# Performance work log

Measured on AMD Instinct MI355X. Metric: run time of the kernel, lower is better.

Reference implementation:

```python
import jax, jax.numpy as jnp
import numpy as np

D_MODEL = 1024
NUM_HEADS = 16
D_HEAD = D_MODEL // NUM_HEADS
BATCH, SEQ, MEM = 2, 1024, 1024
TOT = SEQ + MEM


def setup_inputs() -> dict:
    key = jax.random.key(0)
    ks = jax.random.split(key, 16)
    s = 0.02
    return {
        "x": jax.random.normal(ks[0], (BATCH, SEQ, D_MODEL), jnp.float32),
        "mem": jax.random.normal(ks[1], (BATCH, MEM, D_MODEL), jnp.float32),
        "mask": jnp.zeros((1, 1, SEQ, TOT), jnp.float32),
        "rel_enc": jax.random.normal(ks[2], (TOT, D_MODEL), jnp.float32),
        "Wq": jax.random.normal(ks[3], (D_MODEL, D_MODEL), jnp.float32) * s,
        "bq": jnp.zeros((D_MODEL,), jnp.float32),
        "Wke": jax.random.normal(ks[4], (D_MODEL, D_MODEL), jnp.float32) * s,
        "bke": jnp.zeros((D_MODEL,), jnp.float32),
        "Wkr": jax.random.normal(ks[5], (D_MODEL, D_MODEL), jnp.float32) * s,
        "bkr": jnp.zeros((D_MODEL,), jnp.float32),
        "Wv": jax.random.normal(ks[6], (D_MODEL, D_MODEL), jnp.float32) * s,
        "bv": jnp.zeros((D_MODEL,), jnp.float32),
        "Wo": jax.random.normal(ks[7], (D_MODEL, D_MODEL), jnp.float32) * s,
        "bo": jnp.zeros((D_MODEL,), jnp.float32),
    }


def _split_heads(t, b):
    # (b, s, d_model) -> (b, h, s, d_head)
    return t.reshape(b, -1, NUM_HEADS, D_HEAD).transpose(0, 2, 1, 3)


def _rel_enc_shift(arr):
    # arr: (b, h, l, m) -> Transformer-XL shift trick
    b, h, l, m = arr.shape
    arr = jnp.concatenate([arr, jnp.zeros((b, h, l, 1), arr.dtype)], axis=-1)
    arr = arr.reshape(b, h, l * (m + 1))
    return arr[:, :, l - 1:-1].reshape(b, h, l, m)


def reference(x, mem, mask, rel_enc, Wq, bq, Wke, bke, Wkr, bkr, Wv, bv, Wo, bo):
    b, s, _ = x.shape
    x_tilde = jnp.concatenate([mem, x], axis=1)  # (b, tot, d)
    q = _split_heads(x @ Wq + bq, b)             # (b, h, s, dh)
    k = _split_heads(x_tilde @ Wke + bke, b)     # (b, h, tot, dh)
    v = _split_heads(x_tilde @ Wv + bv, b)       # (b, h, tot, dh)
    A = jnp.einsum("bhsd,bhtd->bhst", q, k)      # content scores
    Q = (rel_enc @ Wkr + bkr).reshape(-1, NUM_HEADS, D_HEAD).transpose(1, 0, 2)  # (h, tot, dh)
    B_hat = jnp.einsum("bhsd,htd->bhst", q, Q)
    B = _rel_enc_shift(B_hat)                    # relative-position scores
    scores = (A + B) / jnp.sqrt(jnp.float32(D_HEAD)) + mask * -1e9
    w = jax.nn.softmax(scores, axis=-1)
    out = jnp.einsum("bhst,bhtd->bhsd", w, v)
    out = out.transpose(0, 2, 1, 3).reshape(b, s, D_MODEL)
    return out @ Wo + bo
```

## Files before the change

kernel.cpp:

```cpp
#include <hip/hip_runtime.h>

typedef unsigned short ushort;
typedef unsigned int uint;
typedef __attribute__((ext_vector_type(8))) short short8;
typedef __attribute__((ext_vector_type(4))) float float4v;

#define D_MODEL 1024
#define NH 16
#define DH 64
#define BATCH 2
#define SEQ 1024
#define MEMLEN 1024
#define TOT 2048

__device__ __forceinline__ float b2f(ushort u) {
  return __uint_as_float(((uint)u) << 16);
}
__device__ __forceinline__ ushort f2b(float f) {
  uint i = __float_as_uint(f);
  uint r = (i + 0x7fffu + ((i >> 16) & 1u)) >> 16;
  return (ushort)r;
}
__device__ __forceinline__ void gld16(const ushort* g, ushort* l) {
  __builtin_amdgcn_global_load_lds(
      (const __attribute__((address_space(1))) void*)g,
      (__attribute__((address_space(3))) void*)l, 16, 0, 0);
}

__global__ __launch_bounds__(256) void concat_cvt_kernel(
    const float* __restrict__ x, const float* __restrict__ mem,
    ushort* __restrict__ xt, ushort* __restrict__ xb) {
  int idx = blockIdx.x * 256 + threadIdx.x;
  int row = idx >> 7;
  int c8 = (idx & 127) << 3;
  int b = row >> 11;
  int i = row & 2047;
  const float* src = (i < MEMLEN) ? &mem[((b << 10) + i) * D_MODEL]
                                  : &x[((b << 10) + (i - MEMLEN)) * D_MODEL];
  float4 f0 = *(const float4*)(&src[c8]);
  float4 f1 = *(const float4*)(&src[c8 + 4]);
  ushort u[8] = {f2b(f0.x), f2b(f0.y), f2b(f0.z), f2b(f0.w),
                 f2b(f1.x), f2b(f1.y), f2b(f1.z), f2b(f1.w)};
  *(uint4*)(&xt[row * D_MODEL + c8]) = *(const uint4*)u;
  if (i >= MEMLEN)
    *(uint4*)(&xb[((b << 10) + (i - MEMLEN)) * D_MODEL + c8]) = *(const uint4*)u;
}

__global__ __launch_bounds__(256) void cvt_kernel(const float* __restrict__ in,
                                                  ushort* __restrict__ out) {
  int idx = blockIdx.x * 256 + threadIdx.x;
  int base = idx << 3;
  float4 f0 = *(const float4*)(&in[base]);
  float4 f1 = *(const float4*)(&in[base + 4]);
  ushort u[8] = {f2b(f0.x), f2b(f0.y), f2b(f0.z), f2b(f0.w),
                 f2b(f1.x), f2b(f1.y), f2b(f1.z), f2b(f1.w)};
  *(uint4*)(&out[base]) = *(const uint4*)u;
}

__global__ __launch_bounds__(256) void maskcvt_kernel(
    const float* __restrict__ in, ushort* __restrict__ out) {
  int idx = blockIdx.x * 256 + threadIdx.x;
  int base = idx << 3;
  float4 f0 = *(const float4*)(&in[base]);
  float4 f1 = *(const float4*)(&in[base + 4]);
  ushort u[8] = {f2b(f0.x * -1e9f), f2b(f0.y * -1e9f), f2b(f0.z * -1e9f),
                 f2b(f0.w * -1e9f), f2b(f1.x * -1e9f), f2b(f1.y * -1e9f),
                 f2b(f1.z * -1e9f), f2b(f1.w * -1e9f)};
  *(uint4*)(&out[base]) = *(const uint4*)u;
}

__global__ __launch_bounds__(256) void transpose_cvt5_kernel(
    const float* __restrict__ W0, const float* __restrict__ W1,
    const float* __restrict__ W2, const float* __restrict__ W3,
    const float* __restrict__ W4, ushort* __restrict__ T0,
    ushort* __restrict__ T1, ushort* __restrict__ T2, ushort* __restrict__ T3,
    ushort* __restrict__ T4) {
  __shared__ ushort tle[32][33];
  const float* W;
  ushort* T;
  switch (blockIdx.z) {
    case 0: W = W0; T = T0; break;
    case 1: W = W1; T = T1; break;
    case 2: W = W2; T = T2; break;
    case 3: W = W3; T = T3; break;
    default: W = W4; T = T4; break;
  }
  const int bx = blockIdx.x * 32, by = blockIdx.y * 32;
  const int tx = threadIdx.x & 31, ty = threadIdx.x >> 5;
#pragma unroll
  for (int j = 0; j < 32; j += 8)
    tle[ty + j][tx] = f2b(W[(by + ty + j) * 1024 + bx + tx]);
  __syncthreads();
#pragma unroll
  for (int j = 0; j < 32; j += 8)
    T[(bx + ty + j) * 1024 + by + tx] = tle[tx][ty + j];
}

__global__ __launch_bounds__(256) void vtrans_kernel(
    const ushort* __restrict__ kv, ushort* __restrict__ vt) {
  __shared__ ushort tle[32][76];
  const int gx = blockIdx.x;
  const int gy = blockIdx.y;
  const int tid = threadIdx.x;
  const int r = tid >> 3, c8 = (tid & 7) * 8;
  *(uint4*)(&tle[r][c8]) =
      *(const uint4*)(&kv[(gx * 32 + r) * 2048 + 1024 + gy * 64 + c8]);
  __syncthreads();
  const int dr = tid >> 2, tc8 = (tid & 3) * 8;
  const int bb = (gx * 32) >> 11, tbase = (gx * 32) & 2047;
  ushort tmp[8];
#pragma unroll
  for (int j = 0; j < 8; ++j) tmp[j] = tle[tc8 + j][dr];
  *(uint4*)(&vt[((bb << 10) + gy * 64 + dr) * 2048 + tbase + tc8]) =
      *(const uint4*)tmp;
}

__global__ __launch_bounds__(256) void gemm128_kernel(
    const ushort* __restrict__ A, const ushort* __restrict__ BT,
    const float* __restrict__ b0, const float* __restrict__ b1,
    ushort* __restrict__ Cout, int M, int N, int K) {
  __shared__ ushort As[128 * 32];
  __shared__ ushort Bs[128 * 32];
  const int m0 = blockIdx.x * 128, n0 = blockIdx.y * 128;
  const int tid = threadIdx.x;
  const int w = tid >> 6, lane = tid & 63, m15 = lane & 15, q4 = lane >> 4;
  const int wm = w & 1, wn = w >> 1;
  float4v acc[4][4] = {};
  const int c0 = tid, c1 = tid + 256;
  const int r0 = c0 >> 2, u0 = (c0 & 3) * 8;
  const int r1 = c1 >> 2, u1 = (c1 & 3) * 8;

  for (int kk = 0; kk < K; kk += 32) {
    __syncthreads();
    gld16(&A[(m0 + r0) * K + kk + u0], &As[c0 * 8]);
    gld16(&A[(m0 + r1) * K + kk + u1], &As[c1 * 8]);
    gld16(&BT[(n0 + r0) * K + kk + u0], &Bs[c0 * 8]);
    gld16(&BT[(n0 + r1) * K + kk + u1], &Bs[c1 * 8]);
    __syncthreads();
    short8 af[4], bf[4];
#pragma unroll
    for (int i = 0; i < 4; ++i)
      af[i] = *(const short8*)(&As[(wm * 64 + i * 16 + m15) * 32 + q4 * 8]);
#pragma unroll
    for (int j = 0; j < 4; ++j)
      bf[j] = *(const short8*)(&Bs[(wn * 64 + j * 16 + m15) * 32 + q4 * 8]);
#pragma unroll
    for (int i = 0; i < 4; ++i)
#pragma unroll
      for (int j = 0; j < 4; ++j)
        acc[i][j] =
            __builtin_amdgcn_mfma_f32_16x16x32_bf16(af[i], bf[j], acc[i][j], 0, 0, 0);
  }
#pragma unroll
  for (int j = 0; j < 4; ++j) {
    int col = n0 + wn * 64 + j * 16 + m15;
    float bv = (col < 1024) ? b0[col] : b1[col - 1024];
    float sc = (col < 1024) ? 0.125f : 1.0f;
#pragma unroll
    for (int i = 0; i < 4; ++i) {
      int rowb = m0 + wm * 64 + i * 16 + q4 * 4;
#pragma unroll
      for (int r = 0; r < 4; ++r)
        Cout[(rowb + r) * N + col] = f2b((acc[i][j][r] + bv) * sc);
    }
  }
}

template <int EPI>
__global__ __launch_bounds__(256) void gemm64_kernel(
    const ushort* __restrict__ A, const ushort* __restrict__ BT0,
    const ushort* __restrict__ BT1, int rowSplit, const float* __restrict__ b0,
    const float* __restrict__ b1, void* __restrict__ Cout, int M, int N, int K) {
  __shared__ ushort As[64 * 32];
  __shared__ ushort Bs[128 * 32];
  const int m0 = blockIdx.x * 64, n0 = blockIdx.y * 128;
  const ushort* BT = (m0 < rowSplit) ? BT0 : BT1;
  const float* bias = (m0 < rowSplit) ? b0 : b1;
  const int tid = threadIdx.x;
  const int w = tid >> 6, lane = tid & 63, m15 = lane & 15, q4 = lane >> 4;
  float4v acc[4][2] = {};
  const int ra = tid >> 2, ua = (tid & 3) * 8;
  const int c0 = tid, c1 = tid + 256;
  const int rb0 = c0 >> 2, ub0 = (c0 & 3) * 8;
  const int rb1 = c1 >> 2, ub1 = (c1 & 3) * 8;

  for (int kk = 0; kk < K; kk += 32) {
    __syncthreads();
    gld16(&A[(m0 + ra) * K + kk + ua], &As[tid * 8]);
    gld16(&BT[(n0 + rb0) * K + kk + ub0], &Bs[c0 * 8]);
    gld16(&BT[(n0 + rb1) * K + kk + ub1], &Bs[c1 * 8]);
    __syncthreads();
    short8 bf[2];
#pragma unroll
    for (int j = 0; j < 2; ++j)
      bf[j] = *(const short8*)(&Bs[(w * 32 + j * 16 + m15) * 32 + q4 * 8]);
#pragma unroll
    for (int i = 0; i < 4; ++i) {
      short8 af = *(const short8*)(&As[(i * 16 + m15) * 32 + q4 * 8]);
#pragma unroll
      for (int j = 0; j < 2; ++j)
        acc[i][j] =
            __builtin_amdgcn_mfma_f32_16x16x32_bf16(af, bf[j], acc[i][j], 0, 0, 0);
    }
  }
#pragma unroll
  for (int j = 0; j < 2; ++j) {
    int col = n0 + w * 32 + j * 16 + m15;
    float bv = bias[col];
#pragma unroll
    for (int i = 0; i < 4; ++i) {
      int rowb = m0 + i * 16 + q4 * 4;
#pragma unroll
      for (int r = 0; r < 4; ++r) {
        float v = acc[i][j][r] + bv;
        if (EPI == 1)
          ((float*)Cout)[(rowb + r) * N + col] = v;
        else
          ((ushort*)Cout)[(rowb + r) * N + col] = f2b(v);
      }
    }
  }
}

__global__ __launch_bounds__(256) void bhat_kernel(
    const ushort* __restrict__ q, const ushort* __restrict__ Qrb,
    ushort* __restrict__ Bh) {
  __shared__ ushort As[2 * 128 * 32];
  __shared__ ushort Bs[2 * 128 * 32];
  const int bs0 = blockIdx.x * 128, u0 = blockIdx.y * 128, h = blockIdx.z;
  const int tid = threadIdx.x;
  const int w = tid >> 6, lane = tid & 63, m15 = lane & 15, q4 = lane >> 4;
  const int wm = w & 1, wn = w >> 1;

#pragma unroll
  for (int c = 0; c < 4; ++c) {
    int unit = c * 256 + tid;
    int row = (unit >> 2) & 127, kh = unit >> 9, cu = unit & 3;
    gld16(&q[(bs0 + row) * 1024 + (h << 6) + kh * 32 + cu * 8], &As[unit * 8]);
    gld16(&Qrb[(u0 + row) * 1024 + (h << 6) + kh * 32 + cu * 8], &Bs[unit * 8]);
  }
  __syncthreads();

  float4v acc[4][4] = {};
#pragma unroll
  for (int kh = 0; kh < 2; ++kh) {
    short8 af[4], bf[4];
#pragma unroll
    for (int i = 0; i < 4; ++i)
      af[i] = *(const short8*)(&As[kh * 4096 + (wm * 64 + i * 16 + m15) * 32 + q4 * 8]);
#pragma unroll
    for (int j = 0; j < 4; ++j)
      bf[j] = *(const short8*)(&Bs[kh * 4096 + (wn * 64 + j * 16 + m15) * 32 + q4 * 8]);
#pragma unroll
    for (int i = 0; i < 4; ++i)
#pragma unroll
      for (int j = 0; j < 4; ++j)
        acc[i][j] =
            __builtin_amdgcn_mfma_f32_16x16x32_bf16(af[i], bf[j], acc[i][j], 0, 0, 0);
  }
  const int b = bs0 >> 10;
  const int outrow0 = ((b << 4) + h) * 1024 + (bs0 & 1023);
#pragma unroll
  for (int j = 0; j < 4; ++j) {
    int col = u0 + wn * 64 + j * 16 + m15;
#pragma unroll
    for (int i = 0; i < 4; ++i) {
      int rowb = outrow0 + wm * 64 + i * 16 + q4 * 4;
#pragma unroll
      for (int r = 0; r < 4; ++r)
        Bh[(rowb + r) * 2048 + col] = f2b(acc[i][j][r] * 0.125f);
    }
  }
}

__global__ __launch_bounds__(256) void attn_kernel(
    const ushort* __restrict__ qb, const ushort* __restrict__ kv,
    const ushort* __restrict__ vt, const ushort* __restrict__ Bh,
    const ushort* __restrict__ maskb, ushort* __restrict__ attn) {
  __shared__ ushort Pp[4][16 * 36];
  __shared__ float comb[2][16][68];
  __shared__ float csum[32];

  const int tid = threadIdx.x;
  const int w = tid >> 6, lane = tid & 63, m15 = lane & 15, q4 = lane >> 4;
  const int st = w & 1, th = w >> 1;
  const int s0w = blockIdx.x * 32 + st * 16;
  const int h = blockIdx.y, b = blockIdx.z;
  const int s_l = q4 * 4;

  const ushort* qp = &qb[((b << 10) + s0w + m15) * 1024 + (h << 6) + q4 * 8];
  const short8 af0 = *(const short8*)qp;
  const short8 af1 = *(const short8*)(qp + 32);

  const ushort* kvb = &kv[((size_t)(b << 11) * 2048) + (h << 6)];
  const ushort* vtb = &vt[((size_t)((b << 10) + (h << 6))) * 2048];
  const int bhbase = ((b << 4) + h) << 21;
  ushort* pw = &Pp[w][0];

  ushort bhr[8];
  auto pre_bh = [&](int t0) {
#pragma unroll
    for (int nt = 0; nt < 2; ++nt)
#pragma unroll
      for (int i = 0; i < 4; ++i) {
        int s = s0w + s_l + i;
        int t = t0 + nt * 16 + m15;
        int u = t - s + 1023;
        int row = (u <= 2047) ? s : (s + 1);
        int uu = (u <= 2047) ? u : (u - 2049);
        ushort v = Bh[bhbase + (row << 11) + uu];
        bhr[nt * 4 + i] = (u == 2048) ? (ushort)0 : v;
      }
  };

  float lsum4[4] = {0.f, 0.f, 0.f, 0.f};
  float4v oacc[4] = {};
  pre_bh(th * 1024);

  for (int ci = 0; ci < 32; ++ci) {
    const int t0 = th * 1024 + ci * 32;
    short8 Kr[2][2], Vr[4];
    ushort mk[8];
#pragma unroll
    for (int nt = 0; nt < 2; ++nt) {
      const ushort* kp = &kvb[(size_t)(t0 + nt * 16 + m15) * 2048 + q4 * 8];
      Kr[nt][0] = *(const short8*)kp;
      Kr[nt][1] = *(const short8*)(kp + 32);
    }
#pragma unroll
    for (int nd = 0; nd < 4; ++nd)
      Vr[nd] = *(const short8*)(&vtb[(size_t)(nd * 16 + m15) * 2048 + t0 + q4 * 8]);
#pragma unroll
    for (int nt = 0; nt < 2; ++nt)
#pragma unroll
      for (int i = 0; i < 4; ++i)
        mk[nt * 4 + i] = maskb[(s0w + s_l + i) * 2048 + t0 + nt * 16 + m15];
    ushort bhc[8];
#pragma unroll
    for (int j = 0; j < 8; ++j) bhc[j] = bhr[j];
    if (ci < 31) pre_bh(t0 + 32);

#pragma unroll
    for (int nt = 0; nt < 2; ++nt) {
      float4v a = {0.f, 0.f, 0.f, 0.f};
      a = __builtin_amdgcn_mfma_f32_16x16x32_bf16(af0, Kr[nt][0], a, 0, 0, 0);
      a = __builtin_amdgcn_mfma_f32_16x16x32_bf16(af1, Kr[nt][1], a, 0, 0, 0);
#pragma unroll
      for (int i = 0; i < 4; ++i) {
        float p = __expf(a[i] + b2f(bhc[nt * 4 + i]) + b2f(mk[nt * 4 + i]));
        lsum4[i] += p;
        pw[(s_l + i) * 36 + nt * 16 + m15] = f2b(p);
      }
    }
    short8 pfr = *(const short8*)(&pw[m15 * 36 + q4 * 8]);
#pragma unroll
    for (int nd = 0; nd < 4; ++nd)
      oacc[nd] = __builtin_amdgcn_mfma_f32_16x16x32_bf16(pfr, Vr[nd], oacc[nd], 0, 0, 0);
  }

#pragma unroll
  for (int i = 0; i < 4; ++i) {
    float v = lsum4[i];
    v += __shfl_xor(v, 1, 64);
    v += __shfl_xor(v, 2, 64);
    v += __shfl_xor(v, 4, 64);
    v += __shfl_xor(v, 8, 64);
    lsum4[i] = v;
  }
  if (th == 1) {
#pragma unroll
    for (int nd = 0; nd < 4; ++nd)
#pragma unroll
      for (int i = 0; i < 4; ++i)
        comb[st][s_l + i][nd * 16 + m15] = oacc[nd][i];
    if (m15 == 0)
#pragma unroll
      for (int i = 0; i < 4; ++i) csum[st * 16 + s_l + i] = lsum4[i];
  }
  __syncthreads();
  if (th == 0) {
#pragma unroll
    for (int i = 0; i < 4; ++i) lsum4[i] += csum[st * 16 + s_l + i];
#pragma unroll
    for (int nd = 0; nd < 4; ++nd)
#pragma unroll
      for (int i = 0; i < 4; ++i) {
        float v = oacc[nd][i] + comb[st][s_l + i][nd * 16 + m15];
        attn[((b << 10) + s0w + s_l + i) * 1024 + (h << 6) + nd * 16 + m15] =
            f2b(v / lsum4[i]);
      }
  }
}

extern "C" void kernel_launch(void* const* d_in, const int* in_sizes, int n_in,
                              void* d_out, int out_size, void* d_ws,
                              size_t ws_size, hipStream_t stream) {
  const float* x = (const float*)d_in[0];
  const float* mem = (const float*)d_in[1];
  const float* mask = (const float*)d_in[2];
  const float* rel = (const float*)d_in[3];
  const float* Wq = (const float*)d_in[4];
  const float* bq = (const float*)d_in[5];
  const float* Wke = (const float*)d_in[6];
  const float* bke = (const float*)d_in[7];
  const float* Wkr = (const float*)d_in[8];
  const float* bkr = (const float*)d_in[9];
  const float* Wv = (const float*)d_in[10];
  const float* bv = (const float*)d_in[11];
  const float* Wo = (const float*)d_in[12];
  const float* bo = (const float*)d_in[13];
  float* out = (float*)d_out;

  ushort* ws = (ushort*)d_ws;
  ushort* xt = ws;
  ushort* xbrel = xt + 4096 * 1024;
  ushort* WqT = xbrel + 4096 * 1024;
  ushort* WkeT = WqT + 1024 * 1024;
  ushort* WvT = WkeT + 1024 * 1024;
  ushort* WkrT = WvT + 1024 * 1024;
  ushort* WoT = WkrT + 1024 * 1024;
  ushort* kv = WoT + 1024 * 1024;
  ushort* qr = kv + 4096 * 2048;
  ushort* attn = qr + 4096 * 1024;
  ushort* maskb = attn + 2048 * 1024;
  ushort* Bh = maskb + 1024 * 2048;
  ushort* relb = xbrel + 2048 * 1024;
  ushort* Qrb = qr + 2048 * 1024;
  ushort* vt = xt;

  concat_cvt_kernel<<<2048, 256, 0, stream>>>(x, mem, xt, xbrel);
  cvt_kernel<<<1024, 256, 0, stream>>>(rel, relb);
  maskcvt_kernel<<<1024, 256, 0, stream>>>(mask, maskb);
  transpose_cvt5_kernel<<<dim3(32, 32, 5), 256, 0, stream>>>(
      Wq, Wke, Wkr, Wv, Wo, WqT, WkeT, WkrT, WvT, WoT);

  gemm128_kernel<<<dim3(32, 16), 256, 0, stream>>>(xt, WkeT, bke, bv, kv,
                                                   4096, 2048, 1024);
  gemm64_kernel<0><<<dim3(64, 8), 256, 0, stream>>>(
      xbrel, WqT, WkrT, 2048, bq, bkr, qr, 4096, 1024, 1024);
  vtrans_kernel<<<dim3(128, 16), 256, 0, stream>>>(kv, vt);

  bhat_kernel<<<dim3(16, 16, 16), 256, 0, stream>>>(qr, Qrb, Bh);

  attn_kernel<<<dim3(SEQ / 32, NH, BATCH), 256, 0, stream>>>(
      qr, kv, vt, Bh, maskb, attn);

  gemm64_kernel<1><<<dim3(32, 8), 256, 0, stream>>>(
      attn, WoT, WoT, 1 << 30, bo, bo, out, 2048, 1024, 1024);
}
```

Measured before the change: 365.9 us.

## Pre-shift relative scores in bhat epilogue and vectorize attention bias/mask loads

The bhat kernel now writes its relative-position scores straight into the shifted (s, t) layout, so the attention kernel no longer does per-element gathered loads with index arithmetic for the Transformer-XL shift. The attention kernel routes QK scores through shared memory as floats, transposing them so each lane owns 8 contiguous t values of one row. That lets it load bias and mask with one 16-byte vector load each and build the P fragment in registers. It also merges the rel and mask conversion kernels into one launch. The bhat epilogue stores become scattered with extra index math, and the zero-position element is handled by a per-lane index check.

```diff
diff --git a/kernel.cpp b/kernel.cpp
--- a/kernel.cpp
+++ b/kernel.cpp
@@ -46,26 +46,24 @@
     *(uint4*)(&xb[((b << 10) + (i - MEMLEN)) * D_MODEL + c8]) = *(const uint4*)u;
 }
 
-__global__ __launch_bounds__(256) void cvt_kernel(const float* __restrict__ in,
-                                                  ushort* __restrict__ out) {
+__global__ __launch_bounds__(256) void cvt2_kernel(
+    const float* __restrict__ rel, const float* __restrict__ mask,
+    ushort* __restrict__ relb, ushort* __restrict__ maskb) {
   int idx = blockIdx.x * 256 + threadIdx.x;
+  const float* in;
+  ushort* out;
+  float sc;
+  if (idx < 262144) {
+    in = rel; out = relb; sc = 1.0f;
+  } else {
+    idx -= 262144; in = mask; out = maskb; sc = -1e9f;
+  }
   int base = idx << 3;
   float4 f0 = *(const float4*)(&in[base]);
   float4 f1 = *(const float4*)(&in[base + 4]);
-  ushort u[8] = {f2b(f0.x), f2b(f0.y), f2b(f0.z), f2b(f0.w),
-                 f2b(f1.x), f2b(f1.y), f2b(f1.z), f2b(f1.w)};
-  *(uint4*)(&out[base]) = *(const uint4*)u;
-}
-
-__global__ __launch_bounds__(256) void maskcvt_kernel(
-    const float* __restrict__ in, ushort* __restrict__ out) {
-  int idx = blockIdx.x * 256 + threadIdx.x;
-  int base = idx << 3;
-  float4 f0 = *(const float4*)(&in[base]);
-  float4 f1 = *(const float4*)(&in[base + 4]);
-  ushort u[8] = {f2b(f0.x * -1e9f), f2b(f0.y * -1e9f), f2b(f0.z * -1e9f),
-                 f2b(f0.w * -1e9f), f2b(f1.x * -1e9f), f2b(f1.y * -1e9f),
-                 f2b(f1.z * -1e9f), f2b(f1.w * -1e9f)};
+  ushort u[8] = {f2b(f0.x * sc), f2b(f0.y * sc), f2b(f0.z * sc),
+                 f2b(f0.w * sc), f2b(f1.x * sc), f2b(f1.y * sc),
+                 f2b(f1.z * sc), f2b(f1.w * sc)};
   *(uint4*)(&out[base]) = *(const uint4*)u;
 }
 
@@ -224,7 +222,7 @@
 
 __global__ __launch_bounds__(256) void bhat_kernel(
     const ushort* __restrict__ q, const ushort* __restrict__ Qrb,
-    ushort* __restrict__ Bh) {
+    ushort* __restrict__ Bsh) {
   __shared__ ushort As[2 * 128 * 32];
   __shared__ ushort Bs[2 * 128 * 32];
   const int bs0 = blockIdx.x * 128, u0 = blockIdx.y * 128, h = blockIdx.z;
@@ -259,34 +257,39 @@
             __builtin_amdgcn_mfma_f32_16x16x32_bf16(af[i], bf[j], acc[i][j], 0, 0, 0);
   }
   const int b = bs0 >> 10;
-  const int outrow0 = ((b << 4) + h) * 1024 + (bs0 & 1023);
+  const size_t base = ((size_t)((b << 4) + h)) << 21;
+  const int sb = (bs0 & 1023) + wm * 64 + q4 * 4;
 #pragma unroll
   for (int j = 0; j < 4; ++j) {
-    int col = u0 + wn * 64 + j * 16 + m15;
+    int u = u0 + wn * 64 + j * 16 + m15;
 #pragma unroll
     for (int i = 0; i < 4; ++i) {
-      int rowb = outrow0 + wm * 64 + i * 16 + q4 * 4;
-#pragma unroll
-      for (int r = 0; r < 4; ++r)
-        Bh[(rowb + r) * 2048 + col] = f2b(acc[i][j][r] * 0.125f);
+#pragma unroll
+      for (int r = 0; r < 4; ++r) {
+        int s = sb + i * 16 + r;
+        int t = u + s - 1023;
+        int row = s;
+        if (t < 0) { row = s - 1; t += 2048; }
+        if (row >= 0)
+          Bsh[base + ((size_t)row << 11) + t] = f2b(acc[i][j][r] * 0.125f);
+      }
     }
   }
 }
 
 __global__ __launch_bounds__(256) void attn_kernel(
     const ushort* __restrict__ qb, const ushort* __restrict__ kv,
-    const ushort* __restrict__ vt, const ushort* __restrict__ Bh,
+    const ushort* __restrict__ vt, const ushort* __restrict__ Bsh,
     const ushort* __restrict__ maskb, ushort* __restrict__ attn) {
-  __shared__ ushort Pp[4][16 * 36];
+  __shared__ float Asc[4][16][36];
   __shared__ float comb[2][16][68];
-  __shared__ float csum[32];
+  __shared__ float csum2[2][32];
 
   const int tid = threadIdx.x;
   const int w = tid >> 6, lane = tid & 63, m15 = lane & 15, q4 = lane >> 4;
   const int st = w & 1, th = w >> 1;
   const int s0w = blockIdx.x * 32 + st * 16;
   const int h = blockIdx.y, b = blockIdx.z;
-  const int s_l = q4 * 4;
 
   const ushort* qp = &qb[((b << 10) + s0w + m15) * 1024 + (h << 6) + q4 * 8];
   const short8 af0 = *(const short8*)qp;
@@ -294,33 +297,18 @@
 
   const ushort* kvb = &kv[((size_t)(b << 11) * 2048) + (h << 6)];
   const ushort* vtb = &vt[((size_t)((b << 10) + (h << 6))) * 2048];
-  const int bhbase = ((b << 4) + h) << 21;
-  ushort* pw = &Pp[w][0];
-
-  ushort bhr[8];
-  auto pre_bh = [&](int t0) {
-#pragma unroll
-    for (int nt = 0; nt < 2; ++nt)
-#pragma unroll
-      for (int i = 0; i < 4; ++i) {
-        int s = s0w + s_l + i;
-        int t = t0 + nt * 16 + m15;
-        int u = t - s + 1023;
-        int row = (u <= 2047) ? s : (s + 1);
-        int uu = (u <= 2047) ? u : (u - 2049);
-        ushort v = Bh[bhbase + (row << 11) + uu];
-        bhr[nt * 4 + i] = (u == 2048) ? (ushort)0 : v;
-      }
-  };
-
-  float lsum4[4] = {0.f, 0.f, 0.f, 0.f};
+  const size_t bsbase = ((size_t)((b << 4) + h)) << 21;
+  float* asc = &Asc[w][0][0];
+
+  const int s_r = s0w + m15;
+  const int tof = q4 * 8;
+
+  float lsum = 0.f;
   float4v oacc[4] = {};
-  pre_bh(th * 1024);
 
   for (int ci = 0; ci < 32; ++ci) {
     const int t0 = th * 1024 + ci * 32;
     short8 Kr[2][2], Vr[4];
-    ushort mk[8];
 #pragma unroll
     for (int nt = 0; nt < 2; ++nt) {
       const ushort* kp = &kvb[(size_t)(t0 + nt * 16 + m15) * 2048 + q4 * 8];
@@ -329,66 +317,66 @@
     }
 #pragma unroll
     for (int nd = 0; nd < 4; ++nd)
-      Vr[nd] = *(const short8*)(&vtb[(size_t)(nd * 16 + m15) * 2048 + t0 + q4 * 8]);
-#pragma unroll
-    for (int nt = 0; nt < 2; ++nt)
-#pragma unroll
-      for (int i = 0; i < 4; ++i)
-        mk[nt * 4 + i] = maskb[(s0w + s_l + i) * 2048 + t0 + nt * 16 + m15];
-    ushort bhc[8];
-#pragma unroll
-    for (int j = 0; j < 8; ++j) bhc[j] = bhr[j];
-    if (ci < 31) pre_bh(t0 + 32);
-
+      Vr[nd] = *(const short8*)(&vtb[(size_t)(nd * 16 + m15) * 2048 + t0 + tof]);
+    uint4 bmv = *(const uint4*)(&Bsh[bsbase + ((size_t)s_r << 11) + t0 + tof]);
+    uint4 mkv = *(const uint4*)(&maskb[(s_r << 11) + t0 + tof]);
+
+    float4v aacc[2];
 #pragma unroll
     for (int nt = 0; nt < 2; ++nt) {
       float4v a = {0.f, 0.f, 0.f, 0.f};
       a = __builtin_amdgcn_mfma_f32_16x16x32_bf16(af0, Kr[nt][0], a, 0, 0, 0);
       a = __builtin_amdgcn_mfma_f32_16x16x32_bf16(af1, Kr[nt][1], a, 0, 0, 0);
-#pragma unroll
-      for (int i = 0; i < 4; ++i) {
-        float p = __expf(a[i] + b2f(bhc[nt * 4 + i]) + b2f(mk[nt * 4 + i]));
-        lsum4[i] += p;
-        pw[(s_l + i) * 36 + nt * 16 + m15] = f2b(p);
-      }
-    }
-    short8 pfr = *(const short8*)(&pw[m15 * 36 + q4 * 8]);
+      aacc[nt] = a;
+    }
+#pragma unroll
+    for (int nt = 0; nt < 2; ++nt)
+#pragma unroll
+      for (int i = 0; i < 4; ++i)
+        asc[(q4 * 4 + i) * 36 + nt * 16 + m15] = aacc[nt][i];
+    float4 a0 = *(const float4*)(&asc[m15 * 36 + tof]);
+    float4 a1 = *(const float4*)(&asc[m15 * 36 + tof + 4]);
+
+    const int jz = s_r + 1025 - t0 - tof;
+    ushort pk[8];
+    const ushort* bm = (const ushort*)&bmv;
+    const ushort* mk = (const ushort*)&mkv;
+#pragma unroll
+    for (int j = 0; j < 8; ++j) {
+      float bv = (j == jz) ? 0.f : b2f(bm[j]);
+      float av = (j < 4) ? ((const float*)&a0)[j] : ((const float*)&a1)[j - 4];
+      float p = __expf(av + bv + b2f(mk[j]));
+      lsum += p;
+      pk[j] = f2b(p);
+    }
+    short8 pfr = *(const short8*)pk;
 #pragma unroll
     for (int nd = 0; nd < 4; ++nd)
       oacc[nd] = __builtin_amdgcn_mfma_f32_16x16x32_bf16(pfr, Vr[nd], oacc[nd], 0, 0, 0);
   }
 
-#pragma unroll
-  for (int i = 0; i < 4; ++i) {
-    float v = lsum4[i];
-    v += __shfl_xor(v, 1, 64);
-    v += __shfl_xor(v, 2, 64);
-    v += __shfl_xor(v, 4, 64);
-    v += __shfl_xor(v, 8, 64);
-    lsum4[i] = v;
-  }
+  lsum += __shfl_xor(lsum, 16, 64);
+  lsum += __shfl_xor(lsum, 32, 64);
+  if (q4 == 0) csum2[th][st * 16 + m15] = lsum;
   if (th == 1) {
 #pragma unroll
     for (int nd = 0; nd < 4; ++nd)
 #pragma unroll
       for (int i = 0; i < 4; ++i)
-        comb[st][s_l + i][nd * 16 + m15] = oacc[nd][i];
-    if (m15 == 0)
-#pragma unroll
-      for (int i = 0; i < 4; ++i) csum[st * 16 + s_l + i] = lsum4[i];
+        comb[st][q4 * 4 + i][nd * 16 + m15] = oacc[nd][i];
   }
   __syncthreads();
   if (th == 0) {
 #pragma unroll
-    for (int i = 0; i < 4; ++i) lsum4[i] += csum[st * 16 + s_l + i];
-#pragma unroll
-    for (int nd = 0; nd < 4; ++nd)
-#pragma unroll
-      for (int i = 0; i < 4; ++i) {
-        float v = oacc[nd][i] + comb[st][s_l + i][nd * 16 + m15];
-        attn[((b << 10) + s0w + s_l + i) * 1024 + (h << 6) + nd * 16 + m15] =
-            f2b(v / lsum4[i]);
+    for (int i = 0; i < 4; ++i) {
+      float ls = csum2[0][st * 16 + q4 * 4 + i] + csum2[1][st * 16 + q4 * 4 + i];
+#pragma unroll
+      for (int nd = 0; nd < 4; ++nd) {
+        float v = oacc[nd][i] + comb[st][q4 * 4 + i][nd * 16 + m15];
+        attn[((b << 10) + s0w + q4 * 4 + i) * 1024 + (h << 6) + nd * 16 + m15] =
+            f2b(v / ls);
       }
+    }
   }
 }
 
@@ -423,14 +411,13 @@
   ushort* qr = kv + 4096 * 2048;
   ushort* attn = qr + 4096 * 1024;
   ushort* maskb = attn + 2048 * 1024;
-  ushort* Bh = maskb + 1024 * 2048;
+  ushort* Bsh = maskb + 1024 * 2048;
   ushort* relb = xbrel + 2048 * 1024;
   ushort* Qrb = qr + 2048 * 1024;
   ushort* vt = xt;
 
   concat_cvt_kernel<<<2048, 256, 0, stream>>>(x, mem, xt, xbrel);
-  cvt_kernel<<<1024, 256, 0, stream>>>(rel, relb);
-  maskcvt_kernel<<<1024, 256, 0, stream>>>(mask, maskb);
+  cvt2_kernel<<<2048, 256, 0, stream>>>(rel, mask, relb, maskb);
   transpose_cvt5_kernel<<<dim3(32, 32, 5), 256, 0, stream>>>(
       Wq, Wke, Wkr, Wv, Wo, WqT, WkeT, WkrT, WvT, WoT);
 
@@ -440,10 +427,10 @@
       xbrel, WqT, WkrT, 2048, bq, bkr, qr, 4096, 1024, 1024);
   vtrans_kernel<<<dim3(128, 16), 256, 0, stream>>>(kv, vt);
 
-  bhat_kernel<<<dim3(16, 16, 16), 256, 0, stream>>>(qr, Qrb, Bh);
+  bhat_kernel<<<dim3(16, 16, 16), 256, 0, stream>>>(qr, Qrb, Bsh);
 
   attn_kernel<<<dim3(SEQ / 32, NH, BATCH), 256, 0, stream>>>(
-      qr, kv, vt, Bh, maskb, attn);
+      qr, kv, vt, Bsh, maskb, attn);
 
   gemm64_kernel<1><<<dim3(32, 8), 256, 0, stream>>>(
       attn, WoT, WoT, 1 << 30, bo, bo, out, 2048, 1024, 1024);
```

Result: slower. 377.9 us (+3.3%).
